# Kernel optimization log

Measured on AMD Instinct MI355X. Metric: run time of the kernel, lower is better.

## Reference

```python
import jax, jax.numpy as jnp
import numpy as np

E = 1024
H = 16
DH = E // H
LN_EPS = 1e-5


def setup_inputs() -> dict:
    key = jax.random.key(0)
    ks = jax.random.split(key, 9)
    B, Lq, Lk = 8, 1024, 1024
    s = 0.02
    return {
        "query": jax.random.normal(ks[0], (B, Lq, E), jnp.float32),
        "key_t": jax.random.normal(ks[1], (B, Lk, E), jnp.float32),
        "value": jax.random.normal(ks[2], (B, Lk, E), jnp.float32),
        "in_proj_w": jax.random.normal(ks[3], (3 * E, E), jnp.float32) * s,
        "in_proj_b": jnp.zeros((3 * E,), jnp.float32),
        "out_proj_w": jax.random.normal(ks[4], (E, E), jnp.float32) * s,
        "out_proj_b": jnp.zeros((E,), jnp.float32),
        "ln_gamma": jnp.ones((E,), jnp.float32),
        "ln_beta": jnp.zeros((E,), jnp.float32),
    }


def _mha_cross(query, key_t, value, in_proj_w, in_proj_b, out_proj_w, out_proj_b,
               ln_gamma, ln_beta):
    B, Lq, _ = query.shape
    Lk = key_t.shape[1]
    wq, wk, wv = in_proj_w[:E], in_proj_w[E:2 * E], in_proj_w[2 * E:]
    bq, bk, bv = in_proj_b[:E], in_proj_b[E:2 * E], in_proj_b[2 * E:]
    # projections (torch Linear: x @ W^T + b)
    q = (query @ wq.T + bq).reshape(B, Lq, H, DH)
    k = (key_t @ wk.T + bk).reshape(B, Lk, H, DH)
    v = (value @ wv.T + bv).reshape(B, Lk, H, DH)
    scale = 1.0 / np.sqrt(DH).astype(np.float32)
    # unfused attention: explicit [B,H,Lq,Lk] scores (need_weights=True path)
    scores = jnp.einsum("bqhd,bkhd->bhqk", q, k) * scale
    probs = jax.nn.softmax(scores, axis=-1)
    attn = jnp.einsum("bhqk,bkhd->bqhd", probs, v).reshape(B, Lq, E)
    attn_out = attn @ out_proj_w.T + out_proj_b
    # averaged attention weights (average_attn_weights=True default)
    attn_weights = probs.mean(axis=1)  # [B, Lq, Lk]
    # residual + LayerNorm
    x = query + attn_out
    mu = x.mean(axis=-1, keepdims=True)
    var = x.var(axis=-1, keepdims=True)
    y = (x - mu) * jax.lax.rsqrt(var + LN_EPS) * ln_gamma + ln_beta
    return y, attn_weights


def reference(query, key_t, value, in_proj_w, in_proj_b, out_proj_w, out_proj_b,
              ln_gamma, ln_beta):
    return _mha_cross(query, key_t, value, in_proj_w, in_proj_b,
                      out_proj_w, out_proj_b, ln_gamma, ln_beta)
```

## Files before the change

kernel.cpp:

```cpp
#include <hip/hip_runtime.h>
#include <stdint.h>

#define E_DIM 1024
#define H_NUM 16
#define B_NUM 8
#define LQ 1024
#define LK 1024
#define MROWS (B_NUM * LQ)

typedef unsigned short u16;
typedef __attribute__((ext_vector_type(8))) short bf16x8;
typedef __attribute__((ext_vector_type(4))) short bf16x4;
typedef __attribute__((ext_vector_type(4))) float f32x4;
typedef bf16x8 __attribute__((may_alias)) bf16x8_ma;
typedef bf16x4 __attribute__((may_alias)) bf16x4_ma;

typedef __attribute__((address_space(1))) const void* gas_ptr;
typedef __attribute__((address_space(3))) void* las_ptr;

__device__ __forceinline__ void gload16(const void* g, void* l) {
  __builtin_amdgcn_global_load_lds((gas_ptr)g, (las_ptr)l, 16, 0, 0);
}

__device__ __forceinline__ u16 f2bf(float f) {
  union { float f; uint32_t u; } c; c.f = f;
  return (u16)((c.u + 0x7FFFu + ((c.u >> 16) & 1u)) >> 16);
}

#define MFMA_BF16(a, b, c) __builtin_amdgcn_mfma_f32_16x16x32_bf16((a), (b), (c), 0, 0, 0)

#define SCALE_Q 0.18033688011112042f

__global__ __launch_bounds__(256) void cvt_f32_bf16(const float* __restrict__ src,
                                                    u16* __restrict__ dst, int n4) {
  int i = blockIdx.x * 256 + threadIdx.x;
  const int stride = gridDim.x * 256;
  for (; i < n4; i += stride) {
    float4 v = ((const float4*)src)[i];
    ushort4 o;
    o.x = f2bf(v.x); o.y = f2bf(v.y); o.z = f2bf(v.z); o.w = f2bf(v.w);
    ((ushort4*)dst)[i] = o;
  }
}

__global__ __launch_bounds__(256) void cvt3_f32_bf16(
    const float* __restrict__ a0, const float* __restrict__ a1, const float* __restrict__ a2,
    u16* __restrict__ o0, u16* __restrict__ o1, u16* __restrict__ o2, int n4) {
  const float* s = (blockIdx.y == 0) ? a0 : (blockIdx.y == 1 ? a1 : a2);
  u16* d = (blockIdx.y == 0) ? o0 : (blockIdx.y == 1 ? o1 : o2);
  int i = blockIdx.x * 256 + threadIdx.x;
  const int stride = gridDim.x * 256;
  for (; i < n4; i += stride) {
    float4 v = ((const float4*)s)[i];
    ushort4 o;
    o.x = f2bf(v.x); o.y = f2bf(v.y); o.z = f2bf(v.z); o.w = f2bf(v.w);
    ((ushort4*)d)[i] = o;
  }
}


#define BAR() __builtin_amdgcn_s_barrier()
#define LGKM0() do { asm volatile("s_waitcnt lgkmcnt(0)" ::: "memory"); \
                     __builtin_amdgcn_sched_barrier(0); } while (0)
#define LGKM8() asm volatile("s_waitcnt lgkmcnt(8)" ::: "memory")
#define VMC(n) asm volatile("s_waitcnt vmcnt(" n ")" ::: "memory")

#define STAGEH(mat, rowbase, kt, ldsoff)                                     \
  { const u16* _s = (mat) + (size_t)(rowbase) * E_DIM + (kt);                \
    gload16(_s + goff0, ldsv + (ldsoff) + wave * 1024);                      \
    gload16(_s + goff1, ldsv + (ldsoff) + 8192 + wave * 1024); }

#define READ_B(db)                                                           \
  _Pragma("unroll") for (int n = 0; n < 4; ++n) {                            \
    const int rgb = wn4 + n;                                                 \
    _Pragma("unroll") for (int ks = 0; ks < 2; ++ks)                         \
      bfr[n][ks] = *(const bf16x8_ma*)(ldsc + 65536 + (db) * 32768 +         \
          ((rgb >> 3) << 14) + (((rgb & 7) * 2 + ks) << 10) + lanebase);     \
  }

#define READ_A(db, q)                                                        \
  _Pragma("unroll") for (int jj = 0; jj < 2; ++jj) {                         \
    const int rga = 4 * (q) + 2 * jj + wm;                                   \
    _Pragma("unroll") for (int ks = 0; ks < 2; ++ks)                         \
      afr[jj][ks] = *(const bf16x8_ma*)(ldsc + (db) * 32768 +                \
          ((rga >> 3) << 14) + (((rga & 7) * 2 + ks) << 10) + lanebase);     \
  }

#define MMA(q)                                                               \
  __builtin_amdgcn_s_setprio(1);                                             \
  _Pragma("unroll") for (int jj = 0; jj < 2; ++jj)                           \
    _Pragma("unroll") for (int n = 0; n < 4; ++n)                            \
      _Pragma("unroll") for (int ks = 0; ks < 2; ++ks)                       \
        acc[2 * (q) + jj][n] =                                               \
            MFMA_BF16(afr[jj][ks], bfr[n][ks], acc[2 * (q) + jj][n]);        \
  __builtin_amdgcn_s_setprio(0);

template <int MODE>
__global__ __launch_bounds__(512, 2) void gemm256(
    const u16* __restrict__ A0, const u16* __restrict__ A1, const u16* __restrict__ A2,
    const u16* __restrict__ W, const float* __restrict__ bias,
    const float* __restrict__ resid,
    u16* __restrict__ outb, float* __restrict__ outf,
    int nwg_n, int nwg_m) {
  __shared__ u16 lds[65536];

  const int tid = threadIdx.x;
  const int wave = tid >> 6, lane = tid & 63;
  const int lr = lane & 15, lg = lane >> 4;
  const int wm = wave >> 2, wn4 = (wave & 3) * 4;

  const int cpx = (int)gridDim.x >> 3;
  const int bid = blockIdx.x;
  const int wg = (bid & 7) * cpx + (bid >> 3);
  const int n_i = wg % nwg_n;
  const int rest = wg / nwg_n;
  const int m_i = rest % nwg_m;
  const int z = rest / nwg_m;
  const int m0 = m_i * 256, n0 = n_i * 256;

  const u16* Az = (z == 0) ? A0 : (z == 1 ? A1 : A2);
  const u16* Wz = W + (size_t)z * E_DIM * E_DIM;
  const float* bs = bias + z * E_DIM;
  const float scale = (MODE == 0 && z == 0) ? SCALE_Q : 1.0f;

  int goff0, goff1;
  {
    const int X0 = wave * 1024 + lane * 16;
    const int L0 = X0 ^ (((X0 >> 9) & 1) << 5);
    goff0 = (((L0 >> 10) >> 1) * 16 + ((L0 >> 6) & 15)) * E_DIM +
            ((L0 >> 10) & 1) * 32 + ((L0 & 63) >> 1);
    const int X1 = 8192 + X0;
    const int L1 = X1 ^ (((X1 >> 9) & 1) << 5);
    goff1 = (((L1 >> 10) >> 1) * 16 + ((L1 >> 6) & 15)) * E_DIM +
            ((L1 >> 10) & 1) * 32 + ((L1 & 63) >> 1);
  }
  const char* ldsc = (const char*)lds;
  char* ldsv = (char*)lds;
  const int lanebase = lr * 64 + ((lg * 16) ^ ((lane & 8) << 2));

  const f32x4 fzero = {0.f, 0.f, 0.f, 0.f};
  f32x4 acc[8][4];
#pragma unroll
  for (int j = 0; j < 8; ++j)
#pragma unroll
    for (int n = 0; n < 4; ++n) acc[j][n] = fzero;

  STAGEH(Az, m0,       0,  0);
  STAGEH(Az, m0 + 128, 0,  16384);
  STAGEH(Wz, n0,       0,  65536);
  STAGEH(Wz, n0 + 128, 0,  65536 + 16384);
  STAGEH(Wz, n0,       64, 65536 + 32768);
  STAGEH(Wz, n0 + 128, 64, 65536 + 32768 + 16384);
  STAGEH(Az, m0,       64, 32768);
  VMC("6");
  BAR();

  bf16x8 bfr[4][2], afr[2][2];
#pragma unroll 1
  for (int i = 0; i < 8; ++i) {
    const int kt2 = i * 128 + 128;
    const bool nl = (i < 7);
    READ_B(0) READ_A(0, 0)
    STAGEH(Az, m0 + 128, i * 128 + 64, 32768 + 16384);
    LGKM8();
    BAR(); LGKM0();
    MMA(0)
    BAR();
    READ_A(0, 1)
    if (nl) STAGEH(Wz, n0, kt2, 65536);
    BAR(); LGKM0();
    MMA(1)
    BAR();
    READ_A(0, 2)
    if (nl) STAGEH(Az, m0, kt2, 0);
    BAR(); LGKM0();
    MMA(2)
    BAR();
    READ_A(0, 3)
    if (nl) {
      STAGEH(Wz, n0 + 128, kt2, 65536 + 16384);
      VMC("6");
    } else {
      VMC("0");
    }
    BAR(); LGKM0();
    MMA(3)
    BAR();
    READ_B(1) READ_A(1, 0)
    if (nl) STAGEH(Az, m0 + 128, kt2, 16384);
    LGKM8();
    BAR(); LGKM0();
    MMA(0)
    BAR();
    READ_A(1, 1)
    if (nl) STAGEH(Wz, n0, kt2 + 64, 65536 + 32768);
    BAR(); LGKM0();
    MMA(1)
    BAR();
    READ_A(1, 2)
    if (nl) STAGEH(Wz, n0 + 128, kt2 + 64, 65536 + 32768 + 16384);
    BAR(); LGKM0();
    MMA(2)
    BAR();
    READ_A(1, 3)
    if (nl) {
      STAGEH(Az, m0, kt2 + 64, 32768);
      VMC("6");
    }
    BAR(); LGKM0();
    MMA(3)
    BAR();
  }

  float bvv[4];
#pragma unroll
  for (int n = 0; n < 4; ++n) bvv[n] = bs[n0 + wn4 * 16 + n * 16 + lr];

  if (MODE == 0) {
    u16* Cb = outb + (size_t)z * (size_t)MROWS * E_DIM;
#pragma unroll
    for (int j = 0; j < 8; ++j) {
      const int rbase = m0 + (2 * j + wm) * 16 + lg * 4;
#pragma unroll
      for (int ii = 0; ii < 4; ++ii) {
        const size_t m = (size_t)(rbase + ii);
#pragma unroll
        for (int n = 0; n < 4; ++n) {
          const int nn = n0 + wn4 * 16 + n * 16 + lr;
          Cb[m * E_DIM + nn] = f2bf((acc[j][n][ii] + bvv[n]) * scale);
        }
      }
    }
  } else {
#pragma unroll
    for (int j = 0; j < 8; ++j) {
      const int rbase = m0 + (2 * j + wm) * 16 + lg * 4;
#pragma unroll
      for (int ii = 0; ii < 4; ++ii) {
        const size_t m = (size_t)(rbase + ii);
#pragma unroll
        for (int n = 0; n < 4; ++n) {
          const int nn = n0 + wn4 * 16 + n * 16 + lr;
          outf[m * E_DIM + nn] = acc[j][n][ii] + bvv[n] + resid[m * E_DIM + nn];
        }
      }
    }
  }
}

__global__ __launch_bounds__(256) void transpose_v(const u16* __restrict__ Vb,
                                                   u16* __restrict__ Vtg) {
  __shared__ u16 T[64 * 264];
  const int tid = threadIdx.x;
  const int b = blockIdx.z, h = blockIdx.y;
  const int k0 = blockIdx.x * 256;
  const int bh = b * H_NUM + h;
  const int krow = tid >> 3;
  const int d0 = (tid & 7) * 8;
  const int jst = krow & 7;
#pragma unroll
  for (int it = 0; it < 8; ++it) {
    const int k = it * 32 + krow;
    bf16x8 v = *(const bf16x8*)&Vb[(size_t)(b * LK + k0 + k) * E_DIM + h * 64 + d0];
#pragma unroll
    for (int jj = 0; jj < 8; ++jj) {
      const int j = (jj + jst) & 7;
      T[(d0 + j) * 264 + k] = (u16)v[j];
    }
  }
  __syncthreads();
  const int d = tid >> 2;
  const int kk0 = (tid & 3) * 64;
  u16* orow = &Vtg[(size_t)(bh * 64 + d) * LK + k0 + kk0];
#pragma unroll
  for (int c = 0; c < 8; ++c)
    *(bf16x8*)&orow[c * 8] = *(const bf16x8*)&T[d * 264 + kk0 + c * 8];
}

__global__ __launch_bounds__(256) void attn_fwd(
    const u16* __restrict__ Qb, const u16* __restrict__ Kb, const u16* __restrict__ Vtg,
    u16* __restrict__ attnb, float* __restrict__ denom) {
  __shared__ u16 Ks[64 * 72];
  __shared__ u16 Vt[64 * 72];
  __shared__ u16 Pw[4][16 * 72];

  const int tid = threadIdx.x;
  const int wave = tid >> 6, lane = tid & 63;
  const int lr = lane & 15, lg = lane >> 4;

  const int bid = blockIdx.x;
  const int wg = (bid & 7) * 256 + (bid >> 3);
  const int qt = wg & 15;
  const int h = (wg >> 4) & 15;
  const int b = wg >> 8;
  const int bh = b * H_NUM + h;
  const int q0 = qt * 64;

  const size_t qoff = (size_t)(b * LQ + q0 + wave * 16 + lr) * E_DIM + h * 64;
  const bf16x8 qf0 = *(const bf16x8*)&Qb[qoff + lg * 8];
  const bf16x8 qf1 = *(const bf16x8*)&Qb[qoff + 32 + lg * 8];

  const f32x4 fzero = {0.f, 0.f, 0.f, 0.f};
  f32x4 ctx[4];
#pragma unroll
  for (int d = 0; d < 4; ++d) ctx[d] = fzero;
  float dnl = 0.f;

  const int sr = tid >> 2;
  const int sc = (tid & 3) * 16;
  const u16* Kg = &Kb[(size_t)(b * LK + sr) * E_DIM + h * 64 + sc];
  const u16* Vg = &Vtg[(size_t)(bh * 64 + sr) * LK + sc];

  bf16x8 kr0 = *(const bf16x8*)(Kg);
  bf16x8 kr1 = *(const bf16x8*)(Kg + 8);
  bf16x8 vr0 = *(const bf16x8*)(Vg);
  bf16x8 vr1 = *(const bf16x8*)(Vg + 8);
  *(bf16x8*)&Ks[sr * 72 + sc] = kr0; *(bf16x8*)&Ks[sr * 72 + sc + 8] = kr1;
  *(bf16x8*)&Vt[sr * 72 + sc] = vr0; *(bf16x8*)&Vt[sr * 72 + sc + 8] = vr1;

  for (int t = 0; t < 16; ++t) {
    __syncthreads();
    if (t < 15) {
      const int k1 = (t + 1) * 64;
      kr0 = *(const bf16x8*)(Kg + (size_t)k1 * E_DIM);
      kr1 = *(const bf16x8*)(Kg + (size_t)k1 * E_DIM + 8);
      vr0 = *(const bf16x8*)(Vg + k1);
      vr1 = *(const bf16x8*)(Vg + k1 + 8);
    }
#pragma unroll
    for (int kf = 0; kf < 4; ++kf) {
      const bf16x8 kb0 = *(const bf16x8*)&Ks[(kf * 16 + lr) * 72 + lg * 8];
      const bf16x8 kb1 = *(const bf16x8*)&Ks[(kf * 16 + lr) * 72 + 32 + lg * 8];
      f32x4 s = fzero;
      s = MFMA_BF16(kb0, qf0, s);
      s = MFMA_BF16(kb1, qf1, s);
      const float p0 = exp2f(s[0]), p1 = exp2f(s[1]);
      const float p2 = exp2f(s[2]), p3 = exp2f(s[3]);
      dnl += (p0 + p1) + (p2 + p3);
      bf16x4 w;
      w[0] = (short)f2bf(p0); w[1] = (short)f2bf(p1);
      w[2] = (short)f2bf(p2); w[3] = (short)f2bf(p3);
      *(bf16x4_ma*)&Pw[wave][lr * 72 + kf * 16 + lg * 4] = w;
    }
    const bf16x8 pa0 = *(const bf16x8_ma*)&Pw[wave][lr * 72 + lg * 8];
    const bf16x8 pa1 = *(const bf16x8_ma*)&Pw[wave][lr * 72 + 32 + lg * 8];
#pragma unroll
    for (int df = 0; df < 4; ++df) {
      const bf16x8 vb0 = *(const bf16x8*)&Vt[(df * 16 + lr) * 72 + lg * 8];
      const bf16x8 vb1 = *(const bf16x8*)&Vt[(df * 16 + lr) * 72 + 32 + lg * 8];
      ctx[df] = MFMA_BF16(pa0, vb0, ctx[df]);
      ctx[df] = MFMA_BF16(pa1, vb1, ctx[df]);
    }
    __syncthreads();
    if (t < 15) {
      *(bf16x8*)&Ks[sr * 72 + sc] = kr0; *(bf16x8*)&Ks[sr * 72 + sc + 8] = kr1;
      *(bf16x8*)&Vt[sr * 72 + sc] = vr0; *(bf16x8*)&Vt[sr * 72 + sc + 8] = vr1;
    }
  }

  dnl += __shfl_xor(dnl, 16, 64);
  dnl += __shfl_xor(dnl, 32, 64);
  if (lane < 16) denom[(size_t)bh * LQ + q0 + wave * 16 + lane] = dnl;
  float dnv[4];
#pragma unroll
  for (int i = 0; i < 4; ++i) dnv[i] = __shfl(dnl, lg * 4 + i, 64);

#pragma unroll
  for (int i = 0; i < 4; ++i) {
    const float inv = 1.0f / dnv[i];
    const int q = q0 + wave * 16 + lg * 4 + i;
    const size_t orow = (size_t)(b * LQ + q) * E_DIM + h * 64;
#pragma unroll
    for (int df = 0; df < 4; ++df)
      attnb[orow + df * 16 + lr] = f2bf(ctx[df][i] * inv);
  }
}

__global__ __launch_bounds__(256) void attn_wts(
    const u16* __restrict__ Qb, const u16* __restrict__ Kb,
    const float* __restrict__ denom, float* __restrict__ aw) {
  __shared__ u16 Ks[128 * 72];

  const int tid = threadIdx.x;
  const int wave = tid >> 6, lane = tid & 63;
  const int lr = lane & 15, lg = lane >> 4;

  const int bid = blockIdx.x;
  const int wg = (bid & 7) * 128 + (bid >> 3);
  const int q0 = (wg & 15) * 64;
  const int k0 = ((wg >> 4) & 7) * 128;
  const int b = wg >> 7;

  const f32x4 fzero = {0.f, 0.f, 0.f, 0.f};
  f32x4 acc[2][4];
#pragma unroll
  for (int t = 0; t < 2; ++t)
#pragma unroll
    for (int f = 0; f < 4; ++f) acc[t][f] = fzero;

  const int sr = tid >> 1;
  const int sc = (tid & 1) * 32;
  const u16* Kg = &Kb[(size_t)(b * LK + k0 + sr) * E_DIM + sc];
  const size_t qbase = (size_t)(b * LQ + q0 + wave * 16 + lr) * E_DIM;
  const size_t dbase = (size_t)(b * H_NUM) * LQ + q0 + wave * 16 + lg * 4;

  bf16x8 r0 = *(const bf16x8*)(Kg);
  bf16x8 r1 = *(const bf16x8*)(Kg + 8);
  bf16x8 r2 = *(const bf16x8*)(Kg + 16);
  bf16x8 r3 = *(const bf16x8*)(Kg + 24);
  *(bf16x8*)&Ks[sr * 72 + sc] = r0;      *(bf16x8*)&Ks[sr * 72 + sc + 8] = r1;
  *(bf16x8*)&Ks[sr * 72 + sc + 16] = r2; *(bf16x8*)&Ks[sr * 72 + sc + 24] = r3;

  for (int h = 0; h < H_NUM; ++h) {
    __syncthreads();
    if (h < 15) {
      const u16* Kn = Kg + (h + 1) * 64;
      r0 = *(const bf16x8*)(Kn);
      r1 = *(const bf16x8*)(Kn + 8);
      r2 = *(const bf16x8*)(Kn + 16);
      r3 = *(const bf16x8*)(Kn + 24);
    }
    const bf16x8 qf0 = *(const bf16x8*)&Qb[qbase + h * 64 + lg * 8];
    const bf16x8 qf1 = *(const bf16x8*)&Qb[qbase + h * 64 + 32 + lg * 8];
    float rd[4];
#pragma unroll
    for (int i = 0; i < 4; ++i)
      rd[i] = 0.0625f / denom[dbase + (size_t)h * LQ + i];

#pragma unroll
    for (int kt = 0; kt < 2; ++kt) {
#pragma unroll
      for (int f = 0; f < 4; ++f) {
        const int row = kt * 64 + f * 16 + lr;
        const bf16x8 kb0 = *(const bf16x8*)&Ks[row * 72 + lg * 8];
        const bf16x8 kb1 = *(const bf16x8*)&Ks[row * 72 + 32 + lg * 8];
        f32x4 s = fzero;
        s = MFMA_BF16(qf0, kb0, s);
        s = MFMA_BF16(qf1, kb1, s);
#pragma unroll
        for (int i = 0; i < 4; ++i)
          acc[kt][f][i] += exp2f(s[i]) * rd[i];
      }
    }
    __syncthreads();
    if (h < 15) {
      *(bf16x8*)&Ks[sr * 72 + sc] = r0;      *(bf16x8*)&Ks[sr * 72 + sc + 8] = r1;
      *(bf16x8*)&Ks[sr * 72 + sc + 16] = r2; *(bf16x8*)&Ks[sr * 72 + sc + 24] = r3;
    }
  }

#pragma unroll
  for (int kt = 0; kt < 2; ++kt)
#pragma unroll
    for (int f = 0; f < 4; ++f)
#pragma unroll
      for (int i = 0; i < 4; ++i) {
        const int q = q0 + wave * 16 + lg * 4 + i;
        aw[(size_t)(b * LQ + q) * LK + k0 + kt * 64 + f * 16 + lr] = acc[kt][f][i];
      }
}

__global__ __launch_bounds__(256) void ln_kernel(float* __restrict__ xy,
                                                 const float* __restrict__ gamma,
                                                 const float* __restrict__ beta) {
  __shared__ float ls[4], ls2[4];
  const int row = blockIdx.x;
  const int tid = threadIdx.x;
  float4* xr = (float4*)(xy + (size_t)row * E_DIM);
  float4 v = xr[tid];
  float s = v.x + v.y + v.z + v.w;
  float s2 = v.x * v.x + v.y * v.y + v.z * v.z + v.w * v.w;
#pragma unroll
  for (int off = 32; off >= 1; off >>= 1) {
    s += __shfl_xor(s, off, 64);
    s2 += __shfl_xor(s2, off, 64);
  }
  const int wave = tid >> 6, lane = tid & 63;
  if (lane == 0) { ls[wave] = s; ls2[wave] = s2; }
  __syncthreads();
  s = ls[0] + ls[1] + ls[2] + ls[3];
  s2 = ls2[0] + ls2[1] + ls2[2] + ls2[3];
  const float mu = s * (1.0f / E_DIM);
  const float var = s2 * (1.0f / E_DIM) - mu * mu;
  const float rs = rsqrtf(var + 1e-5f);
  const float4 g = ((const float4*)gamma)[tid];
  const float4 bt = ((const float4*)beta)[tid];
  float4 o;
  o.x = (v.x - mu) * rs * g.x + bt.x;
  o.y = (v.y - mu) * rs * g.y + bt.y;
  o.z = (v.z - mu) * rs * g.z + bt.z;
  o.w = (v.w - mu) * rs * g.w + bt.w;
  xr[tid] = o;
}

extern "C" void kernel_launch(void* const* d_in, const int* in_sizes, int n_in,
                              void* d_out, int out_size, void* d_ws, size_t ws_size,
                              hipStream_t stream) {
  (void)in_sizes; (void)n_in; (void)out_size; (void)ws_size;
  const float* query     = (const float*)d_in[0];
  const float* key_t     = (const float*)d_in[1];
  const float* value     = (const float*)d_in[2];
  const float* in_proj_b = (const float*)d_in[4];
  const float* out_proj_b = (const float*)d_in[6];
  const float* ln_gamma  = (const float*)d_in[7];
  const float* ln_beta   = (const float*)d_in[8];

  float* y  = (float*)d_out;
  float* aw = y + (size_t)B_NUM * LQ * E_DIM;

  const size_t SZ = (size_t)B_NUM * LQ * E_DIM;
  u16* ws    = (u16*)d_ws;
  u16* Qb    = ws;
  u16* Kb    = ws + SZ;
  u16* Vb    = ws + 2 * SZ;
  u16* attnb = ws + 3 * SZ;
  u16* wqkvb = ws + 4 * SZ;
  u16* woutb = wqkvb + 3 * E_DIM * E_DIM;
  float* denom = (float*)(wqkvb + 4 * (size_t)E_DIM * E_DIM);

  u16* Xq  = (u16*)aw;
  u16* Xk  = Xq + SZ;
  u16* Xv  = (u16*)y;
  u16* Vtg = (u16*)y;

  cvt_f32_bf16<<<3072, 256, 0, stream>>>((const float*)d_in[3], wqkvb, (3 * E_DIM * E_DIM) / 4);
  cvt_f32_bf16<<<1024, 256, 0, stream>>>((const float*)d_in[5], woutb, (E_DIM * E_DIM) / 4);
  cvt3_f32_bf16<<<dim3(2048, 3), 256, 0, stream>>>(query, key_t, value, Xq, Xk, Xv, (int)(SZ / 4));

  gemm256<0><<<384, 512, 0, stream>>>(
      Xq, Xk, Xv, wqkvb, in_proj_b, nullptr, Qb, nullptr, 4, 32);

  transpose_v<<<dim3(4, 16, 8), 256, 0, stream>>>(Vb, Vtg);

  attn_fwd<<<2048, 256, 0, stream>>>(Qb, Kb, Vtg, attnb, denom);

  attn_wts<<<1024, 256, 0, stream>>>(Qb, Kb, denom, aw);

  gemm256<1><<<128, 512, 0, stream>>>(
      attnb, attnb, attnb, woutb, out_proj_b, query, nullptr, y, 4, 32);

  ln_kernel<<<8192, 256, 0, stream>>>(y, ln_gamma, ln_beta);
}
```

Baseline: 294.9 us.

## Restructure attention-weights kernel: drop LDS staging, swap MFMA operands, precompute reciprocal denominators

```diff
diff --git a/kernel.cpp b/kernel.cpp
--- a/kernel.cpp
+++ b/kernel.cpp
@@ -14,6 +14,7 @@
 typedef __attribute__((ext_vector_type(4))) float f32x4;
 typedef bf16x8 __attribute__((may_alias)) bf16x8_ma;
 typedef bf16x4 __attribute__((may_alias)) bf16x4_ma;
+typedef f32x4 __attribute__((may_alias)) f32x4_ma;
 
 typedef __attribute__((address_space(1))) const void* gas_ptr;
 typedef __attribute__((address_space(3))) void* las_ptr;
@@ -279,7 +280,7 @@
 
 __global__ __launch_bounds__(256) void attn_fwd(
     const u16* __restrict__ Qb, const u16* __restrict__ Kb, const u16* __restrict__ Vtg,
-    u16* __restrict__ attnb, float* __restrict__ denom) {
+    u16* __restrict__ attnb, float* __restrict__ rden) {
   __shared__ u16 Ks[64 * 72];
   __shared__ u16 Vt[64 * 72];
   __shared__ u16 Pw[4][16 * 72];
@@ -360,7 +361,7 @@
 
   dnl += __shfl_xor(dnl, 16, 64);
   dnl += __shfl_xor(dnl, 32, 64);
-  if (lane < 16) denom[(size_t)bh * LQ + q0 + wave * 16 + lane] = dnl;
+  if (lane < 16) rden[(size_t)bh * LQ + q0 + wave * 16 + lane] = 0.0625f / dnl;
   float dnv[4];
 #pragma unroll
   for (int i = 0; i < 4; ++i) dnv[i] = __shfl(dnl, lg * 4 + i, 64);
@@ -378,86 +379,51 @@
 
 __global__ __launch_bounds__(256) void attn_wts(
     const u16* __restrict__ Qb, const u16* __restrict__ Kb,
-    const float* __restrict__ denom, float* __restrict__ aw) {
-  __shared__ u16 Ks[128 * 72];
-
+    const float* __restrict__ rden, float* __restrict__ aw) {
   const int tid = threadIdx.x;
   const int wave = tid >> 6, lane = tid & 63;
   const int lr = lane & 15, lg = lane >> 4;
 
   const int bid = blockIdx.x;
-  const int wg = (bid & 7) * 128 + (bid >> 3);
-  const int q0 = (wg & 15) * 64;
-  const int k0 = ((wg >> 4) & 7) * 128;
-  const int b = wg >> 7;
+  const int wg = (bid & 7) * 256 + (bid >> 3);
+  const int kc = wg & 15;
+  const int qt = (wg >> 4) & 15;
+  const int b = wg >> 8;
+  const int q0 = qt * 64;
+  const int kst = kc * 64 + wave * 16;
 
   const f32x4 fzero = {0.f, 0.f, 0.f, 0.f};
-  f32x4 acc[2][4];
-#pragma unroll
-  for (int t = 0; t < 2; ++t)
-#pragma unroll
-    for (int f = 0; f < 4; ++f) acc[t][f] = fzero;
-
-  const int sr = tid >> 1;
-  const int sc = (tid & 1) * 32;
-  const u16* Kg = &Kb[(size_t)(b * LK + k0 + sr) * E_DIM + sc];
-  const size_t qbase = (size_t)(b * LQ + q0 + wave * 16 + lr) * E_DIM;
-  const size_t dbase = (size_t)(b * H_NUM) * LQ + q0 + wave * 16 + lg * 4;
-
-  bf16x8 r0 = *(const bf16x8*)(Kg);
-  bf16x8 r1 = *(const bf16x8*)(Kg + 8);
-  bf16x8 r2 = *(const bf16x8*)(Kg + 16);
-  bf16x8 r3 = *(const bf16x8*)(Kg + 24);
-  *(bf16x8*)&Ks[sr * 72 + sc] = r0;      *(bf16x8*)&Ks[sr * 72 + sc + 8] = r1;
-  *(bf16x8*)&Ks[sr * 72 + sc + 16] = r2; *(bf16x8*)&Ks[sr * 72 + sc + 24] = r3;
-
+  f32x4 acc[4];
+#pragma unroll
+  for (int j = 0; j < 4; ++j) acc[j] = fzero;
+
+  const u16* Kg = &Kb[(size_t)(b * LK + kst + lr) * E_DIM + lg * 8];
+  const u16* Qg = &Qb[(size_t)(b * LQ + q0 + lr) * E_DIM + lg * 8];
+  const float* dg = &rden[(size_t)(b * H_NUM) * LQ + q0 + lr];
+
+#pragma unroll 1
   for (int h = 0; h < H_NUM; ++h) {
-    __syncthreads();
-    if (h < 15) {
-      const u16* Kn = Kg + (h + 1) * 64;
-      r0 = *(const bf16x8*)(Kn);
-      r1 = *(const bf16x8*)(Kn + 8);
-      r2 = *(const bf16x8*)(Kn + 16);
-      r3 = *(const bf16x8*)(Kn + 24);
-    }
-    const bf16x8 qf0 = *(const bf16x8*)&Qb[qbase + h * 64 + lg * 8];
-    const bf16x8 qf1 = *(const bf16x8*)&Qb[qbase + h * 64 + 32 + lg * 8];
+    const bf16x8 kb0 = *(const bf16x8*)(Kg + h * 64);
+    const bf16x8 kb1 = *(const bf16x8*)(Kg + h * 64 + 32);
     float rd[4];
 #pragma unroll
-    for (int i = 0; i < 4; ++i)
-      rd[i] = 0.0625f / denom[dbase + (size_t)h * LQ + i];
-
-#pragma unroll
-    for (int kt = 0; kt < 2; ++kt) {
-#pragma unroll
-      for (int f = 0; f < 4; ++f) {
-        const int row = kt * 64 + f * 16 + lr;
-        const bf16x8 kb0 = *(const bf16x8*)&Ks[row * 72 + lg * 8];
-        const bf16x8 kb1 = *(const bf16x8*)&Ks[row * 72 + 32 + lg * 8];
-        f32x4 s = fzero;
-        s = MFMA_BF16(qf0, kb0, s);
-        s = MFMA_BF16(qf1, kb1, s);
-#pragma unroll
-        for (int i = 0; i < 4; ++i)
-          acc[kt][f][i] += exp2f(s[i]) * rd[i];
-      }
-    }
-    __syncthreads();
-    if (h < 15) {
-      *(bf16x8*)&Ks[sr * 72 + sc] = r0;      *(bf16x8*)&Ks[sr * 72 + sc + 8] = r1;
-      *(bf16x8*)&Ks[sr * 72 + sc + 16] = r2; *(bf16x8*)&Ks[sr * 72 + sc + 24] = r3;
-    }
-  }
-
-#pragma unroll
-  for (int kt = 0; kt < 2; ++kt)
-#pragma unroll
-    for (int f = 0; f < 4; ++f)
-#pragma unroll
-      for (int i = 0; i < 4; ++i) {
-        const int q = q0 + wave * 16 + lg * 4 + i;
-        aw[(size_t)(b * LQ + q) * LK + k0 + kt * 64 + f * 16 + lr] = acc[kt][f][i];
-      }
+    for (int j = 0; j < 4; ++j) rd[j] = dg[(size_t)h * LQ + j * 16];
+#pragma unroll
+    for (int j = 0; j < 4; ++j) {
+      const bf16x8 qf0 = *(const bf16x8*)(Qg + (size_t)(j * 16) * E_DIM + h * 64);
+      const bf16x8 qf1 = *(const bf16x8*)(Qg + (size_t)(j * 16) * E_DIM + h * 64 + 32);
+      f32x4 s = fzero;
+      s = MFMA_BF16(kb0, qf0, s);
+      s = MFMA_BF16(kb1, qf1, s);
+#pragma unroll
+      for (int i = 0; i < 4; ++i)
+        acc[j][i] += exp2f(s[i]) * rd[j];
+    }
+  }
+
+#pragma unroll
+  for (int j = 0; j < 4; ++j)
+    *(f32x4_ma*)&aw[(size_t)(b * LQ + q0 + j * 16 + lr) * LK + kst + lg * 4] = acc[j];
 }
 
 __global__ __launch_bounds__(256) void ln_kernel(float* __restrict__ xy,
@@ -516,7 +482,7 @@
   u16* attnb = ws + 3 * SZ;
   u16* wqkvb = ws + 4 * SZ;
   u16* woutb = wqkvb + 3 * E_DIM * E_DIM;
-  float* denom = (float*)(wqkvb + 4 * (size_t)E_DIM * E_DIM);
+  float* rden = (float*)(wqkvb + 4 * (size_t)E_DIM * E_DIM);
 
   u16* Xq  = (u16*)aw;
   u16* Xk  = Xq + SZ;
@@ -532,9 +498,9 @@
 
   transpose_v<<<dim3(4, 16, 8), 256, 0, stream>>>(Vb, Vtg);
 
-  attn_fwd<<<2048, 256, 0, stream>>>(Qb, Kb, Vtg, attnb, denom);
-
-  attn_wts<<<1024, 256, 0, stream>>>(Qb, Kb, denom, aw);
+  attn_fwd<<<2048, 256, 0, stream>>>(Qb, Kb, Vtg, attnb, rden);
+
+  attn_wts<<<2048, 256, 0, stream>>>(Qb, Kb, rden, aw);
 
   gemm256<1><<<128, 512, 0, stream>>>(
       attnb, attnb, attnb, woutb, out_proj_b, query, nullptr, y, 4, 32);
```

After: 369.0 us. +25.1%, slower.

## Double-buffer K in attention-weights kernel and retile out-projection GEMM to 128x128

Applied to the files above, without the earlier changes.

```diff
diff --git a/kernel.cpp b/kernel.cpp
--- a/kernel.cpp
+++ b/kernel.cpp
@@ -14,6 +14,7 @@
 typedef __attribute__((ext_vector_type(4))) float f32x4;
 typedef bf16x8 __attribute__((may_alias)) bf16x8_ma;
 typedef bf16x4 __attribute__((may_alias)) bf16x4_ma;
+typedef f32x4 __attribute__((may_alias)) f32x4_ma;
 
 typedef __attribute__((address_space(1))) const void* gas_ptr;
 typedef __attribute__((address_space(3))) void* las_ptr;
@@ -248,6 +249,83 @@
   }
 }
 
+__global__ __launch_bounds__(256) void gemm128_out(
+    const u16* __restrict__ A, const u16* __restrict__ W,
+    const float* __restrict__ bias, const float* __restrict__ resid,
+    float* __restrict__ outf, int nwg_n, int nwg_m) {
+  __shared__ u16 As[128 * 64];
+  __shared__ u16 Bs[128 * 64];
+
+  const int tid = threadIdx.x;
+  const int wave = tid >> 6;
+  const int lane = tid & 63;
+  const int lr = lane & 15, lg = lane >> 4;
+  const int wr = wave >> 1, wc = wave & 1;
+
+  const int cpx = (int)gridDim.x >> 3;
+  const int bid = blockIdx.x;
+  const int wg = (bid & 7) * cpx + (bid >> 3);
+  const int n_i = wg % nwg_n;
+  const int m_i = (wg / nwg_n) % nwg_m;
+
+  const int m0 = m_i * 128;
+  const int n0 = n_i * 128;
+
+  const f32x4 fzero = {0.f, 0.f, 0.f, 0.f};
+  f32x4 acc[4][4];
+#pragma unroll
+  for (int a = 0; a < 4; ++a)
+#pragma unroll
+    for (int b = 0; b < 4; ++b) acc[a][b] = fzero;
+
+  const int lrow8 = lane >> 3;
+  const int lcol8 = (lane & 7) * 8;
+
+  for (int kt = 0; kt < E_DIM; kt += 64) {
+#pragma unroll
+    for (int i = 0; i < 4; ++i) {
+      const int seg = i * 4 + wave;
+      gload16(W + (size_t)(n0 + seg * 8 + lrow8) * E_DIM + kt + lcol8, &Bs[seg * 512]);
+      gload16(A + (size_t)(m0 + seg * 8 + lrow8) * E_DIM + kt + lcol8, &As[seg * 512]);
+    }
+    __syncthreads();
+
+#pragma unroll
+    for (int kk = 0; kk < 64; kk += 32) {
+      bf16x8 av[4], bv[4];
+#pragma unroll
+      for (int t = 0; t < 4; ++t)
+        av[t] = *(const bf16x8*)&As[(wr * 64 + t * 16 + lr) * 64 + kk + lg * 8];
+#pragma unroll
+      for (int t = 0; t < 4; ++t)
+        bv[t] = *(const bf16x8*)&Bs[(wc * 64 + t * 16 + lr) * 64 + kk + lg * 8];
+#pragma unroll
+      for (int mi = 0; mi < 4; ++mi)
+#pragma unroll
+        for (int ni = 0; ni < 4; ++ni)
+          acc[mi][ni] = MFMA_BF16(av[mi], bv[ni], acc[mi][ni]);
+    }
+    __syncthreads();
+  }
+
+  float bvv[4];
+#pragma unroll
+  for (int ni = 0; ni < 4; ++ni) bvv[ni] = bias[n0 + wc * 64 + ni * 16 + lr];
+
+#pragma unroll
+  for (int mi = 0; mi < 4; ++mi) {
+#pragma unroll
+    for (int i = 0; i < 4; ++i) {
+      const size_t m = (size_t)(m0 + wr * 64 + mi * 16 + lg * 4 + i);
+#pragma unroll
+      for (int ni = 0; ni < 4; ++ni) {
+        const int n = n0 + wc * 64 + ni * 16 + lr;
+        outf[m * E_DIM + n] = acc[mi][ni][i] + bvv[ni] + resid[m * E_DIM + n];
+      }
+    }
+  }
+}
+
 __global__ __launch_bounds__(256) void transpose_v(const u16* __restrict__ Vb,
                                                    u16* __restrict__ Vtg) {
   __shared__ u16 T[64 * 264];
@@ -279,7 +357,7 @@
 
 __global__ __launch_bounds__(256) void attn_fwd(
     const u16* __restrict__ Qb, const u16* __restrict__ Kb, const u16* __restrict__ Vtg,
-    u16* __restrict__ attnb, float* __restrict__ denom) {
+    u16* __restrict__ attnb, float* __restrict__ rden) {
   __shared__ u16 Ks[64 * 72];
   __shared__ u16 Vt[64 * 72];
   __shared__ u16 Pw[4][16 * 72];
@@ -360,7 +438,7 @@
 
   dnl += __shfl_xor(dnl, 16, 64);
   dnl += __shfl_xor(dnl, 32, 64);
-  if (lane < 16) denom[(size_t)bh * LQ + q0 + wave * 16 + lane] = dnl;
+  if (lane < 16) rden[(size_t)bh * LQ + q0 + wave * 16 + lane] = 0.0625f / dnl;
   float dnv[4];
 #pragma unroll
   for (int i = 0; i < 4; ++i) dnv[i] = __shfl(dnl, lg * 4 + i, 64);
@@ -378,8 +456,8 @@
 
 __global__ __launch_bounds__(256) void attn_wts(
     const u16* __restrict__ Qb, const u16* __restrict__ Kb,
-    const float* __restrict__ denom, float* __restrict__ aw) {
-  __shared__ u16 Ks[128 * 72];
+    const float* __restrict__ rden, float* __restrict__ aw) {
+  __shared__ u16 Ks2[2][128 * 72];
 
   const int tid = threadIdx.x;
   const int wave = tid >> 6, lane = tid & 63;
@@ -401,18 +479,20 @@
   const int sr = tid >> 1;
   const int sc = (tid & 1) * 32;
   const u16* Kg = &Kb[(size_t)(b * LK + k0 + sr) * E_DIM + sc];
-  const size_t qbase = (size_t)(b * LQ + q0 + wave * 16 + lr) * E_DIM;
-  const size_t dbase = (size_t)(b * H_NUM) * LQ + q0 + wave * 16 + lg * 4;
-
-  bf16x8 r0 = *(const bf16x8*)(Kg);
-  bf16x8 r1 = *(const bf16x8*)(Kg + 8);
-  bf16x8 r2 = *(const bf16x8*)(Kg + 16);
-  bf16x8 r3 = *(const bf16x8*)(Kg + 24);
-  *(bf16x8*)&Ks[sr * 72 + sc] = r0;      *(bf16x8*)&Ks[sr * 72 + sc + 8] = r1;
-  *(bf16x8*)&Ks[sr * 72 + sc + 16] = r2; *(bf16x8*)&Ks[sr * 72 + sc + 24] = r3;
+  const size_t qbase = (size_t)(b * LQ + q0 + lr) * E_DIM;
+  const size_t dbase = (size_t)(b * H_NUM) * LQ + q0 + lr;
+
+  {
+    bf16x8 r0 = *(const bf16x8*)(Kg);
+    bf16x8 r1 = *(const bf16x8*)(Kg + 8);
+    bf16x8 r2 = *(const bf16x8*)(Kg + 16);
+    bf16x8 r3 = *(const bf16x8*)(Kg + 24);
+    *(bf16x8*)&Ks2[0][sr * 72 + sc] = r0;      *(bf16x8*)&Ks2[0][sr * 72 + sc + 8] = r1;
+    *(bf16x8*)&Ks2[0][sr * 72 + sc + 16] = r2; *(bf16x8*)&Ks2[0][sr * 72 + sc + 24] = r3;
+  }
 
   for (int h = 0; h < H_NUM; ++h) {
-    __syncthreads();
+    bf16x8 r0, r1, r2, r3;
     if (h < 15) {
       const u16* Kn = Kg + (h + 1) * 64;
       r0 = *(const bf16x8*)(Kn);
@@ -420,44 +500,45 @@
       r2 = *(const bf16x8*)(Kn + 16);
       r3 = *(const bf16x8*)(Kn + 24);
     }
-    const bf16x8 qf0 = *(const bf16x8*)&Qb[qbase + h * 64 + lg * 8];
-    const bf16x8 qf1 = *(const bf16x8*)&Qb[qbase + h * 64 + 32 + lg * 8];
     float rd[4];
 #pragma unroll
-    for (int i = 0; i < 4; ++i)
-      rd[i] = 0.0625f / denom[dbase + (size_t)h * LQ + i];
-
-#pragma unroll
-    for (int kt = 0; kt < 2; ++kt) {
-#pragma unroll
-      for (int f = 0; f < 4; ++f) {
-        const int row = kt * 64 + f * 16 + lr;
-        const bf16x8 kb0 = *(const bf16x8*)&Ks[row * 72 + lg * 8];
-        const bf16x8 kb1 = *(const bf16x8*)&Ks[row * 72 + 32 + lg * 8];
+    for (int j = 0; j < 4; ++j) rd[j] = rden[dbase + (size_t)h * LQ + j * 16];
+
+    __syncthreads();
+
+    const u16* Kbuf = &Ks2[h & 1][0];
+#pragma unroll
+    for (int j = 0; j < 4; ++j) {
+      const bf16x8 qf0 = *(const bf16x8*)&Qb[qbase + (size_t)(j * 16) * E_DIM + h * 64 + lg * 8];
+      const bf16x8 qf1 = *(const bf16x8*)&Qb[qbase + (size_t)(j * 16) * E_DIM + h * 64 + 32 + lg * 8];
+#pragma unroll
+      for (int t = 0; t < 2; ++t) {
+        const int row = wave * 32 + t * 16 + lr;
+        const bf16x8 kb0 = *(const bf16x8*)&Kbuf[row * 72 + lg * 8];
+        const bf16x8 kb1 = *(const bf16x8*)&Kbuf[row * 72 + 32 + lg * 8];
         f32x4 s = fzero;
-        s = MFMA_BF16(qf0, kb0, s);
-        s = MFMA_BF16(qf1, kb1, s);
+        s = MFMA_BF16(kb0, qf0, s);
+        s = MFMA_BF16(kb1, qf1, s);
 #pragma unroll
         for (int i = 0; i < 4; ++i)
-          acc[kt][f][i] += exp2f(s[i]) * rd[i];
+          acc[t][j][i] += __builtin_amdgcn_exp2f(s[i]) * rd[j];
       }
     }
-    __syncthreads();
+
     if (h < 15) {
-      *(bf16x8*)&Ks[sr * 72 + sc] = r0;      *(bf16x8*)&Ks[sr * 72 + sc + 8] = r1;
-      *(bf16x8*)&Ks[sr * 72 + sc + 16] = r2; *(bf16x8*)&Ks[sr * 72 + sc + 24] = r3;
-    }
-  }
-
-#pragma unroll
-  for (int kt = 0; kt < 2; ++kt)
-#pragma unroll
-    for (int f = 0; f < 4; ++f)
-#pragma unroll
-      for (int i = 0; i < 4; ++i) {
-        const int q = q0 + wave * 16 + lg * 4 + i;
-        aw[(size_t)(b * LQ + q) * LK + k0 + kt * 64 + f * 16 + lr] = acc[kt][f][i];
-      }
+      u16* Kw = &Ks2[(h + 1) & 1][0];
+      *(bf16x8*)&Kw[sr * 72 + sc] = r0;      *(bf16x8*)&Kw[sr * 72 + sc + 8] = r1;
+      *(bf16x8*)&Kw[sr * 72 + sc + 16] = r2; *(bf16x8*)&Kw[sr * 72 + sc + 24] = r3;
+    }
+  }
+
+#pragma unroll
+  for (int j = 0; j < 4; ++j) {
+    const size_t orow = (size_t)(b * LQ + q0 + j * 16 + lr) * LK;
+#pragma unroll
+    for (int t = 0; t < 2; ++t)
+      *(f32x4_ma*)&aw[orow + k0 + wave * 32 + t * 16 + lg * 4] = acc[t][j];
+  }
 }
 
 __global__ __launch_bounds__(256) void ln_kernel(float* __restrict__ xy,
@@ -516,7 +597,7 @@
   u16* attnb = ws + 3 * SZ;
   u16* wqkvb = ws + 4 * SZ;
   u16* woutb = wqkvb + 3 * E_DIM * E_DIM;
-  float* denom = (float*)(wqkvb + 4 * (size_t)E_DIM * E_DIM);
+  float* rden = (float*)(wqkvb + 4 * (size_t)E_DIM * E_DIM);
 
   u16* Xq  = (u16*)aw;
   u16* Xk  = Xq + SZ;
@@ -532,12 +613,11 @@
 
   transpose_v<<<dim3(4, 16, 8), 256, 0, stream>>>(Vb, Vtg);
 
-  attn_fwd<<<2048, 256, 0, stream>>>(Qb, Kb, Vtg, attnb, denom);
-
-  attn_wts<<<1024, 256, 0, stream>>>(Qb, Kb, denom, aw);
-
-  gemm256<1><<<128, 512, 0, stream>>>(
-      attnb, attnb, attnb, woutb, out_proj_b, query, nullptr, y, 4, 32);
+  attn_fwd<<<2048, 256, 0, stream>>>(Qb, Kb, Vtg, attnb, rden);
+
+  attn_wts<<<1024, 256, 0, stream>>>(Qb, Kb, rden, aw);
+
+  gemm128_out<<<512, 256, 0, stream>>>(attnb, woutb, out_proj_b, query, y, 8, 64);
 
   ln_kernel<<<8192, 256, 0, stream>>>(y, ln_gamma, ln_beta);
 }
```

Result: no change. 300.0 us (+1.7%).
